# Kernel tuning notes

Measured on AMD Instinct MI355X. Metric: run time of the kernel, lower is better.

The kernel has to match this reference:

```python
import jax, jax.numpy as jnp
import numpy as np

D_EMBED = 64      # per-head dim (module uses d_embed as head dim)
N_HEADS = 8
SCALE = 1.0 / float(np.sqrt(D_EMBED))
ROPE_BASE = 10000.0


def _rope(x):
    # torchtune-style interleaved RoPE. x: [B, S, H, D]
    B, S, H, D = x.shape
    freqs = 1.0 / (ROPE_BASE ** (jnp.arange(0, D, 2, dtype=jnp.float32) / D))  # [D/2]
    ang = jnp.arange(S, dtype=jnp.float32)[:, None] * freqs[None, :]           # [S, D/2]
    cos = jnp.cos(ang)[None, :, None, :]
    sin = jnp.sin(ang)[None, :, None, :]
    x1 = x[..., 0::2]
    x2 = x[..., 1::2]
    return jnp.stack([x1 * cos - x2 * sin, x1 * sin + x2 * cos], axis=-1).reshape(B, S, H, D)


def setup_inputs() -> dict:
    key = jax.random.key(0)
    ks = jax.random.split(key, 5)
    B, S, D, H = 2, 2048, D_EMBED, N_HEADS
    std = 1.0 / np.sqrt(D)
    return {
        "q": jax.random.normal(ks[0], (B, S, D), jnp.float32),
        "Wq": jax.random.normal(ks[1], (H * D, D), jnp.float32) * std,
        "Wk": jax.random.normal(ks[2], (H * D, D), jnp.float32) * std,
        "Wv": jax.random.normal(ks[3], (H * D, D), jnp.float32) * std,
        "Wo": jax.random.normal(ks[4], (D, H * D), jnp.float32) * std,
        "gamma": jnp.ones((H,), jnp.float32),
    }


def reference(q, Wq, Wk, Wv, Wo, gamma):
    B, S, D = q.shape
    H = N_HEADS
    qh = (q @ Wq.T).reshape(B, S, H, D)
    kh = (q @ Wk.T).reshape(B, S, H, D)
    vh = (q @ Wv.T).reshape(B, S, H, D)
    qh = _rope(qh).transpose(0, 2, 1, 3)  # [B,H,S,D]
    kh = _rope(kh).transpose(0, 2, 1, 3)
    vh = vh.transpose(0, 2, 1, 3)
    # RBF attention scores
    qn = jnp.sum(qh * qh, axis=-1, keepdims=True)                 # [B,H,S,1]
    kn = jnp.sum(kh * kh, axis=-1, keepdims=True)                 # [B,H,S,1]
    qk = jnp.einsum('bhsd,bhtd->bhst', qh, kh)                    # [B,H,S,S]
    dist = jnp.maximum(qn - 2.0 * qk + jnp.swapaxes(kn, -2, -1), 0.0)
    scores = jnp.exp(-(gamma[None, :, None, None] * SCALE) * dist)
    causal = jnp.tril(jnp.ones((S, S), dtype=bool))
    scores = jnp.where(causal, scores, 0.0)
    out = jnp.einsum('bhst,bhtd->bhsd', scores, vh)
    out = out.transpose(0, 2, 1, 3).reshape(B, S, H * D)
    return out @ Wo.T
```

## Files before the change

### kernel.cpp

```cpp
#include <hip/hip_runtime.h>
#include <hip/hip_bf16.h>

#define BB 2
#define SS 2048
#define DD 64
#define HH 8
#define HD 512
#define SCALE 0.125f

typedef __bf16 bf16;
typedef __attribute__((ext_vector_type(4))) __bf16 bf16x4;
typedef __attribute__((ext_vector_type(8))) __bf16 bf16x8;
typedef __attribute__((ext_vector_type(4))) float floatx4;

#define PSLOT 2097152

__device__ __forceinline__ floatx4 mfma16(bf16x8 a, bf16x8 b, floatx4 c) {
    return __builtin_amdgcn_mfma_f32_16x16x32_bf16(a, b, c, 0, 0, 0);
}

#define PV_MFMA(ACC, A, B) \
    asm("s_nop 1\n\tv_mfma_f32_16x16x16_bf16 %0, %1, %2, %0" \
        : "+v"(ACC) : "v"(A), "v"(B))

#define MFMA_DRAIN4(A0, A1, A2, A3) \
    asm volatile("s_nop 7\n\ts_nop 7" : "+v"(A0), "+v"(A1), "+v"(A2), "+v"(A3))

#define GLL(G, L) __builtin_amdgcn_global_load_lds( \
    (const __attribute__((address_space(1))) void*)(G), \
    (__attribute__((address_space(3))) void*)(L), 16, 0, 0)

__device__ __forceinline__ bf16x8 load8(const void* base, size_t idx, int f32) {
    if (f32) {
        const float* p = (const float*)base + idx;
        const float4 a = *reinterpret_cast<const float4*>(p);
        const float4 b = *reinterpret_cast<const float4*>(p + 4);
        bf16x8 r;
        r[0] = (bf16)a.x; r[1] = (bf16)a.y; r[2] = (bf16)a.z; r[3] = (bf16)a.w;
        r[4] = (bf16)b.x; r[5] = (bf16)b.y; r[6] = (bf16)b.z; r[7] = (bf16)b.w;
        return r;
    }
    return *reinterpret_cast<const bf16x8*>((const bf16*)base + idx);
}

__device__ __forceinline__ float load1(const void* base, int idx, int f32) {
    return f32 ? ((const float*)base)[idx] : (float)((const bf16*)base)[idx];
}

__global__ __launch_bounds__(256) void proj_rope_kernel(
    const void* __restrict__ q, const void* __restrict__ Wq,
    const void* __restrict__ Wk, const void* __restrict__ Wv,
    const void* __restrict__ gamma,
    bf16* __restrict__ qh, bf16* __restrict__ kh, bf16* __restrict__ vt,
    float* __restrict__ qn, float* __restrict__ kn,
    int* __restrict__ flagw)
{
    const int lane = threadIdx.x & 63;
    const int wid  = blockIdx.x * 4 + (threadIdx.x >> 6);
    if (wid >= 3 * BB * HH * (SS / 64)) return;
    const int l16  = lane & 15;
    const int quad = lane >> 4;

    int hit = 0;
    const unsigned short* qu = (const unsigned short*)q;
#pragma unroll
    for (int i = 0; i < 16; ++i) {
        const unsigned short u = qu[lane + i * 64];
        if (((u >> 7) & 0xFF) >= 134) hit = 1;
    }
    const int f32 = (__ballot(hit) != 0ull) ? 1 : 0;
    if (wid == 0 && lane == 0) *flagw = f32;

    int id = wid;
    const int h   = id % HH; id /= HH;
    const int st4 = id % (SS / 64); id /= (SS / 64);
    const int b   = id % BB; id /= BB;
    const int w   = id;

    const void* W = (w == 0) ? Wq : (w == 1) ? Wk : Wv;
    const size_t bh = (size_t)b * HH + h;

    bf16x8 wb0[4], wb1[4];
#pragma unroll
    for (int t = 0; t < 4; ++t) {
        const size_t wrow = (size_t)(h * 64 + t * 16 + l16) * DD;
        wb0[t] = load8(W, wrow + quad * 8, f32);
        wb1[t] = load8(W, wrow + quad * 8 + 32, f32);
    }

    float frevA[4], frevB[4];
    float ncc = 0.f;
    if (w < 2) {
        ncc = -load1(gamma, h, f32) * SCALE * 1.4426950408889634f;
#pragma unroll
        for (int t = 0; t < 4; ++t) {
            const int dbase = t * 16 + quad * 4;
            frevA[t] = __builtin_amdgcn_exp2f(
                -(float)dbase * (13.2877123795f / 64.0f)) * 0.15915494309f;
            frevB[t] = __builtin_amdgcn_exp2f(
                -(float)(dbase + 2) * (13.2877123795f / 64.0f)) * 0.15915494309f;
        }
    }

    for (int s4 = 0; s4 < 4; ++s4) {
        const int s0 = (st4 * 4 + s4) * 16;
        const size_t qrow = ((size_t)b * SS + s0 + l16) * DD;
        bf16x8 a0 = load8(q, qrow + quad * 8, f32);
        bf16x8 a1 = load8(q, qrow + quad * 8 + 32, f32);

        floatx4 cv[4];
#pragma unroll
        for (int t = 0; t < 4; ++t) {
            floatx4 acc = {0.f, 0.f, 0.f, 0.f};
            if (w < 2) {
                acc = mfma16(wb0[t], a0, acc);
                acc = mfma16(wb1[t], a1, acc);
            } else {
                acc = mfma16(a0, wb0[t], acc);
                acc = mfma16(a1, wb1[t], acc);
            }
            cv[t] = acc;
        }

        if (w < 2) {
            bf16*  dst  = (w == 0) ? qh : kh;
            float* ndst = (w == 0) ? qn : kn;
            const float srowf = (float)(s0 + l16);
            float nacc = 0.f;
            bf16* drow = dst + (bh * SS + s0 + l16) * DD + quad * 4;
#pragma unroll
            for (int t = 0; t < 4; ++t) {
                float revA = srowf * frevA[t]; revA -= floorf(revA);
                float revB = srowf * frevB[t]; revB -= floorf(revB);
                const float snA = __builtin_amdgcn_sinf(revA);
                const float csA = __builtin_amdgcn_cosf(revA);
                const float snB = __builtin_amdgcn_sinf(revB);
                const float csB = __builtin_amdgcn_cosf(revB);
                const float x0 = cv[t][0], x1 = cv[t][1];
                const float x2 = cv[t][2], x3 = cv[t][3];
                const float r0 = x0 * csA - x1 * snA;
                const float r1 = x0 * snA + x1 * csA;
                const float r2 = x2 * csB - x3 * snB;
                const float r3 = x2 * snB + x3 * csB;
                nacc += r0 * r0 + r1 * r1 + r2 * r2 + r3 * r3;
                bf16x4 o; o[0]=(bf16)r0; o[1]=(bf16)r1; o[2]=(bf16)r2; o[3]=(bf16)r3;
                *reinterpret_cast<bf16x4*>(drow + t * 16) = o;
            }
            nacc += __shfl_xor(nacc, 16);
            nacc += __shfl_xor(nacc, 32);
            if (quad == 0) ndst[bh * SS + s0 + l16] = ncc * nacc;
        } else {
            bf16* vrow = vt + ((size_t)bh * 128 + st4 * 4 + s4) * 1024
                       + l16 * 16 + quad * 4;
#pragma unroll
            for (int t = 0; t < 4; ++t) {
                bf16x4 pv;
#pragma unroll
                for (int r = 0; r < 4; ++r) pv[r] = (bf16)cv[t][r];
                *reinterpret_cast<bf16x4*>(vrow + t * 256) = pv;
            }
        }
    }
}

__global__ __launch_bounds__(256) void attn_kernel(
    const bf16* __restrict__ qh, const bf16* __restrict__ kh,
    const bf16* __restrict__ vt, const float* __restrict__ qn,
    const float* __restrict__ kn, const void* __restrict__ gamma,
    bf16* __restrict__ partial, const int* __restrict__ flagp,
    int NU, int U, int pb)
{
    __shared__ __align__(16) char smem[16384];
    const int f32  = *flagp;
    const int tid  = threadIdx.x;
    const int wv   = tid >> 6;
    const int lane = tid & 63;
    const int l16  = lane & 15;
    const int quad = lane >> 4;

    const int xcd  = blockIdx.x & 7;
    int sblk = blockIdx.x >> 3;
    const int half = (sblk >= pb) ? 1 : 0;
    const int bh   = xcd + (half << 3);
    sblk -= half * pb;

    const int j   = sblk / NU;
    const int u   = sblk - j * NU;
    const int B   = 2 * (j + 1);
    const int c0  = u * U;
    const int nA  = (c0 < B) ? (((c0 + U) < B ? (c0 + U) : B) - c0) : 0;
    const int bB  = ((c0 > B ? c0 : B) - B);
    const int slotA = u;
    const int slotB = u - (B / U);
    const int h    = bh & 7;

    const float twocc = 2.0f * load1(gamma, h, f32) * SCALE * 1.4426950408889634f;

    int q4 = (nA > 0) ? j : (31 - j);
    int s0 = (q4 * 4 + wv) * 16;

    const bf16* qb = qh + ((size_t)bh * SS + s0 + l16) * DD;
    bf16x8 aq0 = *reinterpret_cast<const bf16x8*>(qb + quad * 8);
    bf16x8 aq1 = *reinterpret_cast<const bf16x8*>(qb + quad * 8 + 32);
    float qnc_l = qn[(size_t)bh * SS + s0 + l16];

    floatx4 acc0 = {0.f,0.f,0.f,0.f}, acc1 = {0.f,0.f,0.f,0.f};
    floatx4 acc2 = {0.f,0.f,0.f,0.f}, acc3 = {0.f,0.f,0.f,0.f};

    const float* knp   = kn + (size_t)bh * SS + quad * 4;
    const char* kgbase = (const char*)(kh + (size_t)bh * SS * DD);
    const char* vgbase = (const char*)(vt + (size_t)bh * 131072);

    const int jK   = wv * 64 + lane;
    const int keyK = jK >> 3;
    const int cK   = ((jK & 7) - keyK) & 7;
    const int goffK = keyK * 128 + cK * 16;
    const int goffV = jK * 16;
    char* ldsK = smem + wv * 1024;
    char* ldsV = smem + 8192 + wv * 1024;

    const int kro0 = (l16 * 8 + ((quad + l16) & 7)) * 16;
    const int kro1 = (l16 * 8 + ((quad + 4 + l16) & 7)) * 16;
    const int vro  = l16 * 32 + quad * 8;

#define T0_OF(C) (((C) < nA ? (c0 + (C)) : (bB + (C) - nA)) * 32)

#define STORE_O(SLOT, S0) do { \
    bf16* pbp = partial + (size_t)(SLOT) * PSLOT \
              + ((size_t)bh * SS + (S0) + l16) * DD + quad * 4; \
    bf16x4 o_; \
    o_[0]=(bf16)acc0[0]; o_[1]=(bf16)acc0[1]; o_[2]=(bf16)acc0[2]; o_[3]=(bf16)acc0[3]; \
    *reinterpret_cast<bf16x4*>(pbp +  0) = o_; \
    o_[0]=(bf16)acc1[0]; o_[1]=(bf16)acc1[1]; o_[2]=(bf16)acc1[2]; o_[3]=(bf16)acc1[3]; \
    *reinterpret_cast<bf16x4*>(pbp + 16) = o_; \
    o_[0]=(bf16)acc2[0]; o_[1]=(bf16)acc2[1]; o_[2]=(bf16)acc2[2]; o_[3]=(bf16)acc2[3]; \
    *reinterpret_cast<bf16x4*>(pbp + 32) = o_; \
    o_[0]=(bf16)acc3[0]; o_[1]=(bf16)acc3[1]; o_[2]=(bf16)acc3[2]; o_[3]=(bf16)acc3[3]; \
    *reinterpret_cast<bf16x4*>(pbp + 48) = o_; \
} while (0)

    {
        const int t0p = T0_OF(0);
        GLL(kgbase + (size_t)t0p * 128 + goffK, ldsK);
        GLL(vgbase + (size_t)(t0p >> 4) * 2048 + goffV, ldsV);
    }

    int buf = 0;
    for (int c = 0; c < U; ++c) {
        __builtin_amdgcn_s_barrier();

        const int t0 = T0_OF(c);
        const float4 knv0 = *reinterpret_cast<const float4*>(knp + t0);
        const float4 knv1 = *reinterpret_cast<const float4*>(knp + t0 + 16);

        if (c == nA && nA > 0) {
            MFMA_DRAIN4(acc0, acc1, acc2, acc3);
            STORE_O(slotA, s0);
            acc0 = {0.f,0.f,0.f,0.f}; acc1 = {0.f,0.f,0.f,0.f};
            acc2 = {0.f,0.f,0.f,0.f}; acc3 = {0.f,0.f,0.f,0.f};
            q4 = 31 - j;
            s0 = (q4 * 4 + wv) * 16;
            const bf16* qb2 = qh + ((size_t)bh * SS + s0 + l16) * DD;
            aq0 = *reinterpret_cast<const bf16x8*>(qb2 + quad * 8);
            aq1 = *reinterpret_cast<const bf16x8*>(qb2 + quad * 8 + 32);
            qnc_l = qn[(size_t)bh * SS + s0 + l16];
        }

        asm volatile("" ::: "memory");

        const int tn = T0_OF((c + 1 < U) ? (c + 1) : c);
        GLL(kgbase + (size_t)tn * 128 + goffK, ldsK + ((buf ^ 1) << 12));
        GLL(vgbase + (size_t)(tn >> 4) * 2048 + goffV, ldsV + ((buf ^ 1) << 12));

        asm volatile("s_waitcnt vmcnt(4)" ::: "memory");

        const char* Kb = smem + (buf << 12);
        const char* Vb = smem + 8192 + (buf << 12);

        bf16x8 kc0 = *reinterpret_cast<const bf16x8*>(Kb + kro0);
        bf16x8 kc1 = *reinterpret_cast<const bf16x8*>(Kb + kro1);
        bf16x8 kc2 = *reinterpret_cast<const bf16x8*>(Kb + 2048 + kro0);
        bf16x8 kc3 = *reinterpret_cast<const bf16x8*>(Kb + 2048 + kro1);
        bf16x4 v00 = *reinterpret_cast<const bf16x4*>(Vb + vro);
        bf16x4 v01 = *reinterpret_cast<const bf16x4*>(Vb + 512 + vro);
        bf16x4 v02 = *reinterpret_cast<const bf16x4*>(Vb + 1024 + vro);
        bf16x4 v03 = *reinterpret_cast<const bf16x4*>(Vb + 1536 + vro);
        bf16x4 v10 = *reinterpret_cast<const bf16x4*>(Vb + 2048 + vro);
        bf16x4 v11 = *reinterpret_cast<const bf16x4*>(Vb + 2560 + vro);
        bf16x4 v12 = *reinterpret_cast<const bf16x4*>(Vb + 3072 + vro);
        bf16x4 v13 = *reinterpret_cast<const bf16x4*>(Vb + 3584 + vro);

        floatx4 z0 = {0.f,0.f,0.f,0.f};
        z0 = mfma16(kc0, aq0, z0);
        z0 = mfma16(kc1, aq1, z0);
        floatx4 z1 = {0.f,0.f,0.f,0.f};
        z1 = mfma16(kc2, aq0, z1);
        z1 = mfma16(kc3, aq1, z1);

        const float* k0_ = (const float*)&knv0;
        const float* k1_ = (const float*)&knv1;
        const int diag = !(t0 + 31 <= s0);
        const int dq0 = s0 + l16 - t0 - quad * 4;

        bf16x4 p0;
        if (!diag) {
#pragma unroll
            for (int i = 0; i < 4; ++i) {
                float rawA = fmaf(twocc, z0[i], qnc_l + k0_[i]);
                p0[i] = (bf16)__builtin_amdgcn_exp2f(rawA);
            }
        } else {
#pragma unroll
            for (int i = 0; i < 4; ++i) {
                float rawA = fmaf(twocc, z0[i], qnc_l + k0_[i]);
                float eA = __builtin_amdgcn_exp2f(rawA);
                p0[i] = (bf16)((i <= dq0) ? eA : 0.f);
            }
        }
        PV_MFMA(acc0, v00, p0);
        PV_MFMA(acc1, v01, p0);
        PV_MFMA(acc2, v02, p0);
        PV_MFMA(acc3, v03, p0);

        bf16x4 p1;
        if (!diag) {
#pragma unroll
            for (int i = 0; i < 4; ++i) {
                float rawB = fmaf(twocc, z1[i], qnc_l + k1_[i]);
                p1[i] = (bf16)__builtin_amdgcn_exp2f(rawB);
            }
        } else {
            const int dq1 = dq0 - 16;
#pragma unroll
            for (int i = 0; i < 4; ++i) {
                float rawB = fmaf(twocc, z1[i], qnc_l + k1_[i]);
                float eB = __builtin_amdgcn_exp2f(rawB);
                p1[i] = (bf16)((i <= dq1) ? eB : 0.f);
            }
        }
        PV_MFMA(acc0, v10, p1);
        PV_MFMA(acc1, v11, p1);
        PV_MFMA(acc2, v12, p1);
        PV_MFMA(acc3, v13, p1);

        buf ^= 1;
    }

    MFMA_DRAIN4(acc0, acc1, acc2, acc3);
    STORE_O((nA == U) ? slotA : slotB, s0);
#undef STORE_O
#undef T0_OF
}

template <int NACT>
__device__ __forceinline__ floatx4 opj_core(const bf16* __restrict__ partial,
                                            const void* __restrict__ Wo,
                                            int b, int srow, size_t brow,
                                            int f32, int quad) {
    floatx4 acc = {0.f, 0.f, 0.f, 0.f};
#pragma unroll 4
    for (int kk = 0; kk < HD; kk += 32) {
        const int h  = kk >> 6;
        const int d0 = (kk & 63) + quad * 8;
        const bf16* ap = partial + (((size_t)(b * 8 + h)) * SS + srow) * 64 + d0;
        bf16x8 v0 = *reinterpret_cast<const bf16x8*>(ap);
        float u[8];
#pragma unroll
        for (int i = 0; i < 8; ++i) u[i] = (float)v0[i];
#pragma unroll
        for (int s = 1; s < NACT; ++s) {
            bf16x8 vs = *reinterpret_cast<const bf16x8*>(ap + (size_t)s * PSLOT);
#pragma unroll
            for (int i = 0; i < 8; ++i) u[i] += (float)vs[i];
        }
        bf16x8 a;
#pragma unroll
        for (int i = 0; i < 8; ++i) a[i] = (bf16)u[i];
        bf16x8 w = load8(Wo, brow + kk, f32);
        acc = mfma16(a, w, acc);
    }
    return acc;
}

__global__ __launch_bounds__(256) void outproj_kernel(
    const bf16* __restrict__ partial, const void* __restrict__ Wo,
    void* __restrict__ out, const int* __restrict__ flagp, int NU, int U)
{
    const int f32  = *flagp;
    const int ct   = threadIdx.x >> 6;
    const int lane = threadIdx.x & 63;
    const int l16  = lane & 15;
    const int quad = lane >> 4;

    const int g0   = blockIdx.x * 16;
    const int b    = g0 >> 11;
    const int s0   = g0 & (SS - 1);
    const int srow = s0 + l16;
    const size_t brow = (size_t)(ct * 16 + l16) * HD + quad * 8;

    const int q4g = s0 >> 6;
    int nact;
    if (q4g < 16) { const int Bp = 2 * (q4g + 1); nact = (Bp + U - 1) / U; }
    else          { const int Bp = 2 * (32 - q4g); nact = NU - Bp / U; }

    floatx4 acc;
    switch (nact) {
        case 1:  acc = opj_core<1>(partial, Wo, b, srow, brow, f32, quad); break;
        case 2:  acc = opj_core<2>(partial, Wo, b, srow, brow, f32, quad); break;
        case 3:  acc = opj_core<3>(partial, Wo, b, srow, brow, f32, quad); break;
        default: acc = opj_core<4>(partial, Wo, b, srow, brow, f32, quad); break;
    }

#pragma unroll
    for (int r = 0; r < 4; ++r) {
        const size_t o = (size_t)(g0 + quad * 4 + r) * DD + ct * 16 + l16;
        if (f32) ((float*)out)[o] = acc[r];
        else     ((bf16*)out)[o]  = (bf16)acc[r];
    }
}

extern "C" void kernel_launch(void* const* d_in, const int* in_sizes, int n_in,
                              void* d_out, int out_size, void* d_ws, size_t ws_size,
                              hipStream_t stream) {
    const void* q     = d_in[0];
    const void* Wq    = d_in[1];
    const void* Wk    = d_in[2];
    const void* Wv    = d_in[3];
    const void* Wo    = d_in[4];
    const void* gamma = d_in[5];

    char* ws = (char*)d_ws;
    bf16*  qh      = (bf16*)(ws);
    bf16*  kh      = (bf16*)(ws + 4194304);
    bf16*  vt      = (bf16*)(ws + 8388608);
    float* qn      = (float*)(ws + 12582912);
    float* kn      = (float*)(ws + 12713984);
    int*   flag    = (int*)  (ws + 12845056);
    bf16*  partial = (bf16*)(ws + 13631488);

    const size_t base = 13631488ull;
    int NU = (ws_size >= base + 3ull * 4194304) ? 3 : 2;
    const int U  = 66 / NU;
    const int pb = 16 * NU;

    const int nproj = 3 * BB * HH * (SS / 64);
    proj_rope_kernel<<<dim3((nproj + 3) / 4), dim3(256), 0, stream>>>(
        q, Wq, Wk, Wv, gamma, qh, kh, vt, qn, kn, flag);
    attn_kernel<<<dim3(16 * pb), dim3(256), 0, stream>>>(
        qh, kh, vt, qn, kn, gamma, partial, flag, NU, U, pb);
    outproj_kernel<<<dim3(BB * SS / 16), dim3(256), 0, stream>>>(
        partial, Wo, d_out, flag, NU, U);
}
```

Measured before the change: 114.5 us.

## Allow four-way key split with uneven chunks and prefetch key norms

Generalizes the split of each attention row-pair's key range so the 66 chunks can be divided unevenly, which allows NU=4 when the workspace is large enough. This raises the attention grid size and shortens per-block loops, with matching slot and active-partial count logic in the output projection. It also prefetches the next chunk's key norms one iteration ahead and adds a min-blocks-per-CU launch bound of 4. The cost is more partial buffers for outproj to read and sum, plus extra index arithmetic.

```diff
diff --git a/kernel.cpp b/kernel.cpp
--- a/kernel.cpp
+++ b/kernel.cpp
@@ -163,12 +163,12 @@
     }
 }
 
-__global__ __launch_bounds__(256) void attn_kernel(
+__global__ __launch_bounds__(256, 4) void attn_kernel(
     const bf16* __restrict__ qh, const bf16* __restrict__ kh,
     const bf16* __restrict__ vt, const float* __restrict__ qn,
     const float* __restrict__ kn, const void* __restrict__ gamma,
     bf16* __restrict__ partial, const int* __restrict__ flagp,
-    int NU, int U, int pb)
+    int NU, int pb)
 {
     __shared__ __align__(16) char smem[16384];
     const int f32  = *flagp;
@@ -187,11 +187,21 @@
     const int j   = sblk / NU;
     const int u   = sblk - j * NU;
     const int B   = 2 * (j + 1);
-    const int c0  = u * U;
-    const int nA  = (c0 < B) ? (((c0 + U) < B ? (c0 + U) : B) - c0) : 0;
-    const int bB  = ((c0 > B ? c0 : B) - B);
+
+    const int U0   = 66 / NU;
+    const int rem  = 66 - U0 * NU;
+    const int c0   = u * U0 + ((u < rem) ? u : rem);
+    const int clen = U0 + (u < rem ? 1 : 0);
+    int F = 0;
+#pragma unroll
+    for (int v = 0; v < 6; ++v) {
+        if (v < NU) F += (((v + 1) * U0 + (((v + 1) < rem) ? (v + 1) : rem)) <= B);
+    }
+
+    const int nA  = (c0 < B) ? (((B - c0) < clen) ? (B - c0) : clen) : 0;
+    const int bB  = (c0 > B) ? (c0 - B) : 0;
     const int slotA = u;
-    const int slotB = u - (B / U);
+    const int slotB = u - F;
     const int h    = bh & 7;
 
     const float twocc = 2.0f * load1(gamma, h, f32) * SCALE * 1.4426950408889634f;
@@ -239,19 +249,17 @@
     *reinterpret_cast<bf16x4*>(pbp + 48) = o_; \
 } while (0)
 
-    {
-        const int t0p = T0_OF(0);
-        GLL(kgbase + (size_t)t0p * 128 + goffK, ldsK);
-        GLL(vgbase + (size_t)(t0p >> 4) * 2048 + goffV, ldsV);
-    }
+    const int t0p = T0_OF(0);
+    float4 knv0 = *reinterpret_cast<const float4*>(knp + t0p);
+    float4 knv1 = *reinterpret_cast<const float4*>(knp + t0p + 16);
+    GLL(kgbase + (size_t)t0p * 128 + goffK, ldsK);
+    GLL(vgbase + (size_t)(t0p >> 4) * 2048 + goffV, ldsV);
 
     int buf = 0;
-    for (int c = 0; c < U; ++c) {
+    for (int c = 0; c < clen; ++c) {
         __builtin_amdgcn_s_barrier();
 
         const int t0 = T0_OF(c);
-        const float4 knv0 = *reinterpret_cast<const float4*>(knp + t0);
-        const float4 knv1 = *reinterpret_cast<const float4*>(knp + t0 + 16);
 
         if (c == nA && nA > 0) {
             MFMA_DRAIN4(acc0, acc1, acc2, acc3);
@@ -268,7 +276,9 @@
 
         asm volatile("" ::: "memory");
 
-        const int tn = T0_OF((c + 1 < U) ? (c + 1) : c);
+        const int tn = T0_OF((c + 1 < clen) ? (c + 1) : c);
+        float4 knn0 = *reinterpret_cast<const float4*>(knp + tn);
+        float4 knn1 = *reinterpret_cast<const float4*>(knp + tn + 16);
         GLL(kgbase + (size_t)tn * 128 + goffK, ldsK + ((buf ^ 1) << 12));
         GLL(vgbase + (size_t)(tn >> 4) * 2048 + goffV, ldsV + ((buf ^ 1) << 12));
 
@@ -343,11 +353,12 @@
         PV_MFMA(acc2, v12, p1);
         PV_MFMA(acc3, v13, p1);
 
+        knv0 = knn0; knv1 = knn1;
         buf ^= 1;
     }
 
     MFMA_DRAIN4(acc0, acc1, acc2, acc3);
-    STORE_O((nA == U) ? slotA : slotB, s0);
+    STORE_O((nA == clen) ? slotA : slotB, s0);
 #undef STORE_O
 #undef T0_OF
 }
@@ -384,7 +395,7 @@
 
 __global__ __launch_bounds__(256) void outproj_kernel(
     const bf16* __restrict__ partial, const void* __restrict__ Wo,
-    void* __restrict__ out, const int* __restrict__ flagp, int NU, int U)
+    void* __restrict__ out, const int* __restrict__ flagp, int NU)
 {
     const int f32  = *flagp;
     const int ct   = threadIdx.x >> 6;
@@ -398,10 +409,23 @@
     const int srow = s0 + l16;
     const size_t brow = (size_t)(ct * 16 + l16) * HD + quad * 8;
 
+    const int U0  = 66 / NU;
+    const int rem = 66 - U0 * NU;
     const int q4g = s0 >> 6;
-    int nact;
-    if (q4g < 16) { const int Bp = 2 * (q4g + 1); nact = (Bp + U - 1) / U; }
-    else          { const int Bp = 2 * (32 - q4g); nact = NU - Bp / U; }
+    int nact = 0;
+    if (q4g < 16) {
+        const int Bp = 2 * (q4g + 1);
+#pragma unroll
+        for (int v = 0; v < 6; ++v)
+            if (v < NU) nact += ((v * U0 + ((v < rem) ? v : rem)) < Bp);
+    } else {
+        const int Bp = 2 * (32 - q4g);
+        int F = 0;
+#pragma unroll
+        for (int v = 0; v < 6; ++v)
+            if (v < NU) F += (((v + 1) * U0 + (((v + 1) < rem) ? (v + 1) : rem)) <= Bp);
+        nact = NU - F;
+    }
 
     floatx4 acc;
     switch (nact) {
@@ -439,15 +463,17 @@
     bf16*  partial = (bf16*)(ws + 13631488);
 
     const size_t base = 13631488ull;
-    int NU = (ws_size >= base + 3ull * 4194304) ? 3 : 2;
-    const int U  = 66 / NU;
+    int NU;
+    if      (ws_size >= base + 4ull * 4194304) NU = 4;
+    else if (ws_size >= base + 3ull * 4194304) NU = 3;
+    else                                       NU = 2;
     const int pb = 16 * NU;
 
     const int nproj = 3 * BB * HH * (SS / 64);
     proj_rope_kernel<<<dim3((nproj + 3) / 4), dim3(256), 0, stream>>>(
         q, Wq, Wk, Wv, gamma, qh, kh, vt, qn, kn, flag);
     attn_kernel<<<dim3(16 * pb), dim3(256), 0, stream>>>(
-        qh, kh, vt, qn, kn, gamma, partial, flag, NU, U, pb);
+        qh, kh, vt, qn, kn, gamma, partial, flag, NU, pb);
     outproj_kernel<<<dim3(BB * SS / 16), dim3(256), 0, stream>>>(
-        partial, Wo, d_out, flag, NU, U);
-}
+        partial, Wo, d_out, flag, NU);
+}
```

New measurement: 120.3 us. 5.1% more time.
